# Optimization experiments

Measured on AMD Instinct MI355X. Metric: run time of the kernel, lower is better.

Reference implementation:

```python
import jax, jax.numpy as jnp
import numpy as np

PS = 2      # patch_size
TOPK = 3    # topk


def setup_inputs() -> dict:
    key = jax.random.key(0)
    x = jax.random.normal(key, (8, 128, 64, 64), dtype=jnp.float32)
    alpha = jnp.asarray(5.0, dtype=jnp.float32)  # nn.Parameter alpha
    return {"x": x, "alpha": alpha}


def _forward(x, alpha):
    ps = PS
    b, c, h, w = x.shape
    nph, npw = h // ps, w // ps
    npatch = nph * npw
    pa = ps * ps
    # F.normalize(p=2, dim=-3) with torch eps=1e-12
    norm = jnp.maximum(jnp.sqrt(jnp.sum(x * x, axis=1, keepdims=True)), 1e-12)
    x = x / norm
    # patchify -> [b, c, npatch, patch_area] (patches h-major, pixels row-major)
    xp = x.reshape(b, c, nph, ps, npw, ps).transpose(0, 1, 2, 4, 3, 5)
    xp = xp.reshape(b, c, npatch, pa)
    diag_idx = jnp.arange(ps) * (ps + 1)  # [0, 3] for ps=2
    # gather diagonal pixels of each patch -> [b, ps, npatch, c]
    xd = xp[:, :, :, diag_idx].transpose(0, 3, 2, 1)
    # patch correlation matmul -> [b, ps, npatch, npatch]
    corr = jnp.einsum('bpnc,bpmc->bpnm', xd, xd)
    avg = jnp.mean(corr, axis=1, keepdims=True)
    s = jnp.concatenate([corr, avg], axis=1)  # [b, ps+1, npatch, npatch]
    # ZeroWindow gaussian mask (rat_s=0.05); channel index = patch center (r,c)
    sr, sc = 0.05 * nph, 0.05 * npw
    rr = jnp.arange(nph, dtype=jnp.float32)
    cc = jnp.arange(npw, dtype=jnp.float32)
    cent_r, cent_c = jnp.meshgrid(rr, cc, indexing='ij')
    cent_r = cent_r.reshape(npatch)
    cent_c = cent_c.reshape(npatch)
    gr = jnp.exp(-(rr[None, :] - cent_r[:, None]) ** 2 / (2.0 * sr * sr))  # [npatch, nph]
    gc = jnp.exp(-(cc[None, :] - cent_c[:, None]) ** 2 / (2.0 * sc * sc))  # [npatch, npw]
    mask = (1.0 - gr[:, :, None] * gc[:, None, :]).reshape(npatch, npatch)
    s = s * mask[None, None]
    a = s * alpha
    # double (row + col) softmax
    s = jax.nn.softmax(a, axis=-1) * jax.nn.softmax(a, axis=-2)
    # expand avg channel to all patch pixels, scatter diagonal channels back
    new_x = jnp.broadcast_to(s[:, -1:], (b, pa, npatch, npatch))
    new_x = new_x.at[:, diag_idx].set(s[:, :ps])
    # un-patchify second npatch axis to spatial [b, npatch, h, w]
    y = jnp.swapaxes(new_x, 1, 3)  # [b, npatch, npatch, pa]
    y = y.reshape(b, npatch, nph, npw, ps, ps).transpose(0, 1, 2, 4, 3, 5)
    y = y.reshape(b, npatch, h, w)
    # topk over the npatch axis (dim=-3)
    vals = jax.lax.top_k(jnp.moveaxis(y, 1, -1), TOPK)[0]  # [b, h, w, k]
    return jnp.moveaxis(vals, -1, 1)  # [b, k, h, w]


def reference(x, alpha):
    return _forward(x, alpha)
```

## Files before the change

kernel.cpp:

```cpp
#include <hip/hip_runtime.h>
#include <hip/hip_bf16.h>
#include <math.h>

#define NB 8
#define NC 128
#define NH 64
#define NW 64
#define NP 1024
#define TWO_SIG2 5.12f
#define LOG2E 1.44269504089f

static const size_t PSUM_OFF_B = 0;
static const size_t PBUF_OFF_B = (size_t)NB * 3 * 4 * NP * 4;
static const size_t XD_OFF_B   = PBUF_OFF_B + (size_t)NB * NP * 3 * 4 * 3 * 4;

typedef __bf16 bf16x8 __attribute__((ext_vector_type(8)));
typedef float f32x4 __attribute__((ext_vector_type(4)));

#define INSERT3(v, A, Bq, Cq)                          \
  {                                                    \
    const float _na = fmaxf(A, (v));                   \
    const float _nb = __builtin_amdgcn_fmed3f(A, Bq, (v)); \
    Cq = __builtin_amdgcn_fmed3f(Bq, Cq, (v));         \
    A = _na;                                           \
    Bq = _nb;                                          \
  }

#define MERGE3(a0, a1, a2, b0, b1, b2)       \
  {                                          \
    const float _x1 = fmaxf(a0, b0);         \
    const float _y1 = fminf(a0, b0);         \
    const float _x2 = fmaxf(a1, b1);         \
    const float _z  = fmaxf(a2, b2);         \
    a0 = _x1;                                \
    a1 = fmaxf(_y1, _x2);                    \
    a2 = fmaxf(fminf(_y1, _x2), _z);         \
  }

__global__ __launch_bounds__(256) void k1_norm(const float* __restrict__ x,
                                               __hip_bfloat16* __restrict__ xd) {
  __shared__ __align__(16) float tile[NC * 65];
  const int chunk = blockIdx.x;
  const int p = blockIdx.y;
  const int b = blockIdx.z;
  const int t = threadIdx.x;
  const int pix = t & 63;
  const int cw = t >> 6;
  const int nbase = chunk * 64;

  {
    const int n = nbase + pix;
    const int i = ((n >> 5) << 1) + p;
    const int jf = (n & 31);
    const float* xb = x + (size_t)b * NC * NH * NW + (size_t)i * NW;
    for (int cc = 0; cc < 32; ++cc) {
      const int c = (cc << 2) + cw;
      const float2 v2 = ((const float2*)(xb + (size_t)c * NH * NW))[jf];
      tile[c * 65 + pix] = (p == 0) ? v2.x : v2.y;
    }
  }
  __syncthreads();

  const int lane = t & 63;
  const int w = t >> 6;
  for (int pg = 0; pg < 16; ++pg) {
    const int pixel = (pg << 2) + w;
    const float v0 = tile[lane * 65 + pixel];
    const float v1 = tile[(lane + 64) * 65 + pixel];
    float ss = v0 * v0 + v1 * v1;
#pragma unroll
    for (int m = 32; m >= 1; m >>= 1) ss += __shfl_xor(ss, m, 64);
    const float inv = 1.0f / fmaxf(sqrtf(ss), 1e-12f);
    __hip_bfloat16* xr = xd + ((size_t)((b * 2 + p) * NP) + nbase + pixel) * NC;
    xr[lane] = __float2bfloat16(v0 * inv);
    xr[lane + 64] = __float2bfloat16(v1 * inv);
  }
}

__global__ __launch_bounds__(256) void k2_sums(const ushort* __restrict__ xd,
                                               const float* __restrict__ alpha_p,
                                               float* __restrict__ psum) {
  __shared__ __align__(16) __bf16 As[2][64 * 136];
  __shared__ __align__(16) __bf16 Bs[2][64 * 136];
  const int t = threadIdx.x;
  const float K = (*alpha_p) * LOG2E;
  const float Cm = -(LOG2E / TWO_SIG2);

  const int cchunk = blockIdx.x;
  const int rowtile = blockIdx.y;
  const int b = blockIdx.z;
  const int i0 = rowtile << 6;
  const int jb = cchunk << 8;

#pragma unroll
  for (int pl = 0; pl < 2; ++pl) {
    const float4* ga = (const float4*)(xd + ((size_t)(b * 2 + pl) * NP + i0) * NC);
#pragma unroll
    for (int it = 0; it < 4; ++it) {
      const int f = (it << 8) + t;
      const int r = f >> 4, q = f & 15;
      *(float4*)(&As[pl][r * 136 + q * 8]) = ga[f];
    }
  }

  const int wave = t >> 6;
  const int lane = t & 63;
  const int lrow = lane & 15;
  const int kq = lane >> 4;

  const int n0 = i0 + wave * 16 + kq * 4;
  const float rnf = (float)(n0 >> 5);
  const float cn0 = (float)(n0 & 31);

  float sums[3][4];
#pragma unroll
  for (int ch = 0; ch < 3; ++ch)
#pragma unroll
    for (int reg = 0; reg < 4; ++reg) sums[ch][reg] = 0.f;

  for (int sc = 0; sc < 4; ++sc) {
    const int j0 = jb + (sc << 6);
    __syncthreads();
#pragma unroll
    for (int pl = 0; pl < 2; ++pl) {
      const float4* gb = (const float4*)(xd + ((size_t)(b * 2 + pl) * NP + j0) * NC);
#pragma unroll
      for (int it = 0; it < 4; ++it) {
        const int f = (it << 8) + t;
        const int r = f >> 4, q = f & 15;
        *(float4*)(&Bs[pl][r * 136 + q * 8]) = gb[f];
      }
    }
    __syncthreads();

    f32x4 acc[2][4];
#pragma unroll
    for (int pl = 0; pl < 2; ++pl)
#pragma unroll
      for (int ct = 0; ct < 4; ++ct)
#pragma unroll
        for (int u = 0; u < 4; ++u) acc[pl][ct][u] = 0.f;

#pragma unroll
    for (int kc = 0; kc < 4; ++kc) {
      const int kk = kc * 32 + (kq << 3);
      const bf16x8 a0 = *(const bf16x8*)(&As[0][(wave * 16 + lrow) * 136 + kk]);
      const bf16x8 a1 = *(const bf16x8*)(&As[1][(wave * 16 + lrow) * 136 + kk]);
#pragma unroll
      for (int ct = 0; ct < 4; ++ct) {
        const bf16x8 b0 = *(const bf16x8*)(&Bs[0][(ct * 16 + lrow) * 136 + kk]);
        const bf16x8 b1 = *(const bf16x8*)(&Bs[1][(ct * 16 + lrow) * 136 + kk]);
        acc[0][ct] = __builtin_amdgcn_mfma_f32_16x16x32_bf16(a0, b0, acc[0][ct], 0, 0, 0);
        acc[1][ct] = __builtin_amdgcn_mfma_f32_16x16x32_bf16(a1, b1, acc[1][ct], 0, 0, 0);
      }
    }

#pragma unroll
    for (int ct = 0; ct < 4; ++ct) {
      const int m = j0 + ct * 16 + lrow;
      const float rmf = (float)(m >> 5);
      const float cmf = (float)(m & 31);
      const float dr = rnf - rmf;
      const float dr2 = dr * dr;
#pragma unroll
      for (int reg = 0; reg < 4; ++reg) {
        const float dc = cn0 + (float)reg - cmf;
        const float d2 = fmaf(dc, dc, dr2);
        const float em = __builtin_amdgcn_exp2f(d2 * Cm);
        const float fm2 = fmaf(-em, K, K);
        const float g0 = fm2 * acc[0][ct][reg];
        const float g1 = fm2 * acc[1][ct][reg];
        sums[0][reg] += __builtin_amdgcn_exp2f(g0);
        sums[1][reg] += __builtin_amdgcn_exp2f(g1);
        sums[2][reg] += __builtin_amdgcn_exp2f(0.5f * (g0 + g1));
      }
    }
  }

#pragma unroll
  for (int off = 1; off < 16; off <<= 1)
#pragma unroll
    for (int ch = 0; ch < 3; ++ch)
#pragma unroll
      for (int reg = 0; reg < 4; ++reg)
        sums[ch][reg] += __shfl_xor(sums[ch][reg], off, 64);

  if (lrow == 0) {
#pragma unroll
    for (int ch = 0; ch < 3; ++ch)
#pragma unroll
      for (int reg = 0; reg < 4; ++reg) {
        const int n = i0 + wave * 16 + kq * 4 + reg;
        psum[(((size_t)b * 3 + ch) * 4 + cchunk) * NP + n] = sums[ch][reg];
      }
  }
}

__global__ __launch_bounds__(256) void k4_topk(const ushort* __restrict__ xd,
                                               const float* __restrict__ alpha_p,
                                               const float* __restrict__ psum,
                                               float* __restrict__ pbuf) {
  __shared__ __align__(16) __bf16 As[2][64 * 136];
  __shared__ __align__(16) __bf16 Bs[2][64 * 136];
  __shared__ float rsr[3][64];
  __shared__ float nlc[3][256];
  const int t = threadIdx.x;
  const float K = (*alpha_p) * LOG2E;
  const float Cm = -(LOG2E / TWO_SIG2);

  const int cchunk = blockIdx.x;
  const int rowtile = blockIdx.y;
  const int b = blockIdx.z;
  const int i0 = rowtile << 6;
  const int jb = cchunk << 8;

  if (t < 192) {
    const int ch = t >> 6, r = t & 63;
    const float* pp = psum + ((size_t)b * 3 + ch) * 4 * NP + i0 + r;
    rsr[ch][r] = 1.0f / (pp[0] + pp[NP] + pp[2 * NP] + pp[3 * NP]);
  }
#pragma unroll
  for (int ch = 0; ch < 3; ++ch) {
    const float* pp = psum + ((size_t)b * 3 + ch) * 4 * NP + jb + t;
    nlc[ch][t] = -__builtin_amdgcn_logf(pp[0] + pp[NP] + pp[2 * NP] + pp[3 * NP]);
  }

#pragma unroll
  for (int pl = 0; pl < 2; ++pl) {
    const float4* ga = (const float4*)(xd + ((size_t)(b * 2 + pl) * NP + i0) * NC);
#pragma unroll
    for (int it = 0; it < 4; ++it) {
      const int f = (it << 8) + t;
      const int r = f >> 4, q = f & 15;
      *(float4*)(&As[pl][r * 136 + q * 8]) = ga[f];
    }
  }

  const int wave = t >> 6;
  const int lane = t & 63;
  const int lrow = lane & 15;
  const int kq = lane >> 4;

  const int n0 = i0 + wave * 16 + kq * 4;
  const float rnf = (float)(n0 >> 5);
  const float cn0 = (float)(n0 & 31);

  float tA[3][4], tB[3][4], tC[3][4];
#pragma unroll
  for (int ch = 0; ch < 3; ++ch)
#pragma unroll
    for (int reg = 0; reg < 4; ++reg) {
      tA[ch][reg] = -3.0e38f; tB[ch][reg] = -3.0e38f; tC[ch][reg] = -3.0e38f;
    }

  for (int sc = 0; sc < 4; ++sc) {
    const int j0 = jb + (sc << 6);
    __syncthreads();
#pragma unroll
    for (int pl = 0; pl < 2; ++pl) {
      const float4* gb = (const float4*)(xd + ((size_t)(b * 2 + pl) * NP + j0) * NC);
#pragma unroll
      for (int it = 0; it < 4; ++it) {
        const int f = (it << 8) + t;
        const int r = f >> 4, q = f & 15;
        *(float4*)(&Bs[pl][r * 136 + q * 8]) = gb[f];
      }
    }
    __syncthreads();

    f32x4 acc[2][4];
#pragma unroll
    for (int pl = 0; pl < 2; ++pl)
#pragma unroll
      for (int ct = 0; ct < 4; ++ct)
#pragma unroll
        for (int u = 0; u < 4; ++u) acc[pl][ct][u] = 0.f;

#pragma unroll
    for (int kc = 0; kc < 4; ++kc) {
      const int kk = kc * 32 + (kq << 3);
      const bf16x8 a0 = *(const bf16x8*)(&As[0][(wave * 16 + lrow) * 136 + kk]);
      const bf16x8 a1 = *(const bf16x8*)(&As[1][(wave * 16 + lrow) * 136 + kk]);
#pragma unroll
      for (int ct = 0; ct < 4; ++ct) {
        const bf16x8 b0 = *(const bf16x8*)(&Bs[0][(ct * 16 + lrow) * 136 + kk]);
        const bf16x8 b1 = *(const bf16x8*)(&Bs[1][(ct * 16 + lrow) * 136 + kk]);
        acc[0][ct] = __builtin_amdgcn_mfma_f32_16x16x32_bf16(a0, b0, acc[0][ct], 0, 0, 0);
        acc[1][ct] = __builtin_amdgcn_mfma_f32_16x16x32_bf16(a1, b1, acc[1][ct], 0, 0, 0);
      }
    }

#pragma unroll
    for (int ct = 0; ct < 4; ++ct) {
      const int mc = sc * 64 + ct * 16 + lrow;
      const int m = jb + mc;
      const float rmf = (float)(m >> 5);
      const float cmf = (float)(m & 31);
      const float dr = rnf - rmf;
      const float dr2 = dr * dr;
      const float nl0 = nlc[0][mc];
      const float nl1 = nlc[1][mc];
      const float nl2 = nlc[2][mc];
#pragma unroll
      for (int reg = 0; reg < 4; ++reg) {
        const float dc = cn0 + (float)reg - cmf;
        const float d2 = fmaf(dc, dc, dr2);
        const float em = __builtin_amdgcn_exp2f(d2 * Cm);
        const float fm2 = fmaf(-em, K, K);
        const float f2 = fm2 + fm2;
        const float a0 = acc[0][ct][reg];
        const float a1 = acc[1][ct][reg];
        const float t0 = fmaf(f2, a0, nl0);
        const float t1 = fmaf(f2, a1, nl1);
        const float t2 = fmaf(fm2, a0 + a1, nl2);
        INSERT3(t0, tA[0][reg], tB[0][reg], tC[0][reg]);
        INSERT3(t1, tA[1][reg], tB[1][reg], tC[1][reg]);
        INSERT3(t2, tA[2][reg], tB[2][reg], tC[2][reg]);
      }
    }
  }

#pragma unroll
  for (int off = 1; off < 16; off <<= 1)
#pragma unroll
    for (int ch = 0; ch < 3; ++ch)
#pragma unroll
      for (int reg = 0; reg < 4; ++reg) {
        const float b0 = __shfl_xor(tA[ch][reg], off, 64);
        const float b1 = __shfl_xor(tB[ch][reg], off, 64);
        const float b2 = __shfl_xor(tC[ch][reg], off, 64);
        MERGE3(tA[ch][reg], tB[ch][reg], tC[ch][reg], b0, b1, b2);
      }

  if (lrow == 0) {
#pragma unroll
    for (int ch = 0; ch < 3; ++ch)
#pragma unroll
      for (int reg = 0; reg < 4; ++reg) {
        const int nr = wave * 16 + kq * 4 + reg;
        const int n = i0 + nr;
        const float irn = rsr[ch][nr];
        const size_t base = ((((size_t)b * NP + n) * 3 + ch) * 4 + cchunk) * 3;
        pbuf[base + 0] = __builtin_amdgcn_exp2f(tA[ch][reg]) * irn;
        pbuf[base + 1] = __builtin_amdgcn_exp2f(tB[ch][reg]) * irn;
        pbuf[base + 2] = __builtin_amdgcn_exp2f(tC[ch][reg]) * irn;
      }
  }
}

__global__ __launch_bounds__(256) void k5_merge(const float* __restrict__ pbuf,
                                                float* __restrict__ out) {
  const int tau = blockIdx.x * 256 + threadIdx.x;
  const int b = tau >> 10;
  const int n = tau & (NP - 1);
  const int rn = n >> 5, cn = n & 31;

  float f0[3], f1[3], f2[3];
#pragma unroll
  for (int ch = 0; ch < 3; ++ch) {
    const size_t base = (((size_t)tau * 3 + ch) * 4) * 3;
    f0[ch] = pbuf[base + 0];
    f1[ch] = pbuf[base + 1];
    f2[ch] = pbuf[base + 2];
#pragma unroll
    for (int p = 1; p < 4; ++p) {
      const float b0 = pbuf[base + p * 3 + 0];
      const float b1 = pbuf[base + p * 3 + 1];
      const float b2 = pbuf[base + p * 3 + 2];
      MERGE3(f0[ch], f1[ch], f2[ch], b0, b1, b2);
    }
  }

  float* ob = out + (size_t)b * 3 * (NH * NW);
  const int i00 = ((rn << 1) * NW) + (cn << 1);
#pragma unroll
  for (int tt = 0; tt < 3; ++tt) {
    float* op = ob + (size_t)tt * (NH * NW);
    const float r0 = (tt == 0) ? f0[0] : (tt == 1) ? f1[0] : f2[0];
    const float r1 = (tt == 0) ? f0[1] : (tt == 1) ? f1[1] : f2[1];
    const float r2 = (tt == 0) ? f0[2] : (tt == 1) ? f1[2] : f2[2];
    op[i00] = r0;
    op[i00 + NW + 1] = r1;
    op[i00 + 1] = r2;
    op[i00 + NW] = r2;
  }
}

extern "C" void kernel_launch(void* const* d_in, const int* in_sizes, int n_in,
                              void* d_out, int out_size, void* d_ws, size_t ws_size,
                              hipStream_t stream) {
  const float* x = (const float*)d_in[0];
  const float* alpha = (const float*)d_in[1];
  float* out = (float*)d_out;
  char* ws = (char*)d_ws;

  float* psum = (float*)(ws + PSUM_OFF_B);
  float* pbuf = (float*)(ws + PBUF_OFF_B);
  __hip_bfloat16* xd = (__hip_bfloat16*)(ws + XD_OFF_B);

  k1_norm<<<dim3(16, 2, NB), 256, 0, stream>>>(x, xd);
  k2_sums<<<dim3(4, 16, NB), 256, 0, stream>>>((const ushort*)xd, alpha, psum);
  k4_topk<<<dim3(4, 16, NB), 256, 0, stream>>>((const ushort*)xd, alpha, psum, pbuf);
  k5_merge<<<dim3(32), 256, 0, stream>>>(pbuf, out);
}
```

Baseline: 104.7 us.

## Fuse softmax-sum and topk kernels with grid barrier, keep logits in registers

Merges the row-sum kernel and the topk kernel into one persistent launch. A software grid-wide atomic barrier separates the phases, and each block keeps its masked correlation logits for the second phase in registers (128 floats per thread), so the bf16 GEMM and mask exponentials are not recomputed and the B tiles are not reloaded. This removes a launch and half the MFMA/exp work. The cost is much higher register pressure under launch_bounds(256,2), and the barrier depends on all 512 blocks being co-resident, which is what the bounded spin-timeout guards against.

```diff
diff --git a/kernel.cpp b/kernel.cpp
--- a/kernel.cpp
+++ b/kernel.cpp
@@ -9,10 +9,12 @@
 #define NP 1024
 #define TWO_SIG2 5.12f
 #define LOG2E 1.44269504089f
+#define NBLK 512u
 
 static const size_t PSUM_OFF_B = 0;
 static const size_t PBUF_OFF_B = (size_t)NB * 3 * 4 * NP * 4;
 static const size_t XD_OFF_B   = PBUF_OFF_B + (size_t)NB * NP * 3 * 4 * 3 * 4;
+static const size_t BAR_OFF_B  = XD_OFF_B + (size_t)NB * 2 * NP * NC * 2;
 
 typedef __bf16 bf16x8 __attribute__((ext_vector_type(8)));
 typedef float f32x4 __attribute__((ext_vector_type(4)));
@@ -38,12 +40,16 @@
   }
 
 __global__ __launch_bounds__(256) void k1_norm(const float* __restrict__ x,
-                                               __hip_bfloat16* __restrict__ xd) {
+                                               __hip_bfloat16* __restrict__ xd,
+                                               unsigned* __restrict__ bar) {
   __shared__ __align__(16) float tile[NC * 65];
   const int chunk = blockIdx.x;
   const int p = blockIdx.y;
   const int b = blockIdx.z;
   const int t = threadIdx.x;
+  if (chunk == 0 && p == 0 && b == 0 && t == 0) {
+    __hip_atomic_store(bar, 0u, __ATOMIC_RELAXED, __HIP_MEMORY_SCOPE_AGENT);
+  }
   const int pix = t & 63;
   const int cw = t >> 6;
   const int nbase = chunk * 64;
@@ -77,129 +83,11 @@
   }
 }
 
-__global__ __launch_bounds__(256) void k2_sums(const ushort* __restrict__ xd,
-                                               const float* __restrict__ alpha_p,
-                                               float* __restrict__ psum) {
-  __shared__ __align__(16) __bf16 As[2][64 * 136];
-  __shared__ __align__(16) __bf16 Bs[2][64 * 136];
-  const int t = threadIdx.x;
-  const float K = (*alpha_p) * LOG2E;
-  const float Cm = -(LOG2E / TWO_SIG2);
-
-  const int cchunk = blockIdx.x;
-  const int rowtile = blockIdx.y;
-  const int b = blockIdx.z;
-  const int i0 = rowtile << 6;
-  const int jb = cchunk << 8;
-
-#pragma unroll
-  for (int pl = 0; pl < 2; ++pl) {
-    const float4* ga = (const float4*)(xd + ((size_t)(b * 2 + pl) * NP + i0) * NC);
-#pragma unroll
-    for (int it = 0; it < 4; ++it) {
-      const int f = (it << 8) + t;
-      const int r = f >> 4, q = f & 15;
-      *(float4*)(&As[pl][r * 136 + q * 8]) = ga[f];
-    }
-  }
-
-  const int wave = t >> 6;
-  const int lane = t & 63;
-  const int lrow = lane & 15;
-  const int kq = lane >> 4;
-
-  const int n0 = i0 + wave * 16 + kq * 4;
-  const float rnf = (float)(n0 >> 5);
-  const float cn0 = (float)(n0 & 31);
-
-  float sums[3][4];
-#pragma unroll
-  for (int ch = 0; ch < 3; ++ch)
-#pragma unroll
-    for (int reg = 0; reg < 4; ++reg) sums[ch][reg] = 0.f;
-
-  for (int sc = 0; sc < 4; ++sc) {
-    const int j0 = jb + (sc << 6);
-    __syncthreads();
-#pragma unroll
-    for (int pl = 0; pl < 2; ++pl) {
-      const float4* gb = (const float4*)(xd + ((size_t)(b * 2 + pl) * NP + j0) * NC);
-#pragma unroll
-      for (int it = 0; it < 4; ++it) {
-        const int f = (it << 8) + t;
-        const int r = f >> 4, q = f & 15;
-        *(float4*)(&Bs[pl][r * 136 + q * 8]) = gb[f];
-      }
-    }
-    __syncthreads();
-
-    f32x4 acc[2][4];
-#pragma unroll
-    for (int pl = 0; pl < 2; ++pl)
-#pragma unroll
-      for (int ct = 0; ct < 4; ++ct)
-#pragma unroll
-        for (int u = 0; u < 4; ++u) acc[pl][ct][u] = 0.f;
-
-#pragma unroll
-    for (int kc = 0; kc < 4; ++kc) {
-      const int kk = kc * 32 + (kq << 3);
-      const bf16x8 a0 = *(const bf16x8*)(&As[0][(wave * 16 + lrow) * 136 + kk]);
-      const bf16x8 a1 = *(const bf16x8*)(&As[1][(wave * 16 + lrow) * 136 + kk]);
-#pragma unroll
-      for (int ct = 0; ct < 4; ++ct) {
-        const bf16x8 b0 = *(const bf16x8*)(&Bs[0][(ct * 16 + lrow) * 136 + kk]);
-        const bf16x8 b1 = *(const bf16x8*)(&Bs[1][(ct * 16 + lrow) * 136 + kk]);
-        acc[0][ct] = __builtin_amdgcn_mfma_f32_16x16x32_bf16(a0, b0, acc[0][ct], 0, 0, 0);
-        acc[1][ct] = __builtin_amdgcn_mfma_f32_16x16x32_bf16(a1, b1, acc[1][ct], 0, 0, 0);
-      }
-    }
-
-#pragma unroll
-    for (int ct = 0; ct < 4; ++ct) {
-      const int m = j0 + ct * 16 + lrow;
-      const float rmf = (float)(m >> 5);
-      const float cmf = (float)(m & 31);
-      const float dr = rnf - rmf;
-      const float dr2 = dr * dr;
-#pragma unroll
-      for (int reg = 0; reg < 4; ++reg) {
-        const float dc = cn0 + (float)reg - cmf;
-        const float d2 = fmaf(dc, dc, dr2);
-        const float em = __builtin_amdgcn_exp2f(d2 * Cm);
-        const float fm2 = fmaf(-em, K, K);
-        const float g0 = fm2 * acc[0][ct][reg];
-        const float g1 = fm2 * acc[1][ct][reg];
-        sums[0][reg] += __builtin_amdgcn_exp2f(g0);
-        sums[1][reg] += __builtin_amdgcn_exp2f(g1);
-        sums[2][reg] += __builtin_amdgcn_exp2f(0.5f * (g0 + g1));
-      }
-    }
-  }
-
-#pragma unroll
-  for (int off = 1; off < 16; off <<= 1)
-#pragma unroll
-    for (int ch = 0; ch < 3; ++ch)
-#pragma unroll
-      for (int reg = 0; reg < 4; ++reg)
-        sums[ch][reg] += __shfl_xor(sums[ch][reg], off, 64);
-
-  if (lrow == 0) {
-#pragma unroll
-    for (int ch = 0; ch < 3; ++ch)
-#pragma unroll
-      for (int reg = 0; reg < 4; ++reg) {
-        const int n = i0 + wave * 16 + kq * 4 + reg;
-        psum[(((size_t)b * 3 + ch) * 4 + cchunk) * NP + n] = sums[ch][reg];
-      }
-  }
-}
-
-__global__ __launch_bounds__(256) void k4_topk(const ushort* __restrict__ xd,
-                                               const float* __restrict__ alpha_p,
-                                               const float* __restrict__ psum,
-                                               float* __restrict__ pbuf) {
+__global__ __launch_bounds__(256, 2) void k24_fused(const ushort* __restrict__ xd,
+                                                    const float* __restrict__ alpha_p,
+                                                    float* __restrict__ psum,
+                                                    float* __restrict__ pbuf,
+                                                    unsigned* __restrict__ bar) {
   __shared__ __align__(16) __bf16 As[2][64 * 136];
   __shared__ __align__(16) __bf16 Bs[2][64 * 136];
   __shared__ float rsr[3][64];
@@ -214,6 +102,126 @@
   const int i0 = rowtile << 6;
   const int jb = cchunk << 8;
 
+#pragma unroll
+  for (int pl = 0; pl < 2; ++pl) {
+    const float4* ga = (const float4*)(xd + ((size_t)(b * 2 + pl) * NP + i0) * NC);
+#pragma unroll
+    for (int it = 0; it < 4; ++it) {
+      const int f = (it << 8) + t;
+      const int r = f >> 4, q = f & 15;
+      *(float4*)(&As[pl][r * 136 + q * 8]) = ga[f];
+    }
+  }
+
+  const int wave = t >> 6;
+  const int lane = t & 63;
+  const int lrow = lane & 15;
+  const int kq = lane >> 4;
+
+  const int n0 = i0 + wave * 16 + kq * 4;
+  const float rnf = (float)(n0 >> 5);
+  const float cn0 = (float)(n0 & 31);
+
+  f32x4 g0v[4][4];
+  f32x4 g1v[4][4];
+#pragma unroll
+  for (int sc = 0; sc < 4; ++sc)
+#pragma unroll
+    for (int ct = 0; ct < 4; ++ct)
+#pragma unroll
+      for (int u = 0; u < 4; ++u) { g0v[sc][ct][u] = 0.f; g1v[sc][ct][u] = 0.f; }
+
+  float sums[3][4];
+#pragma unroll
+  for (int ch = 0; ch < 3; ++ch)
+#pragma unroll
+    for (int reg = 0; reg < 4; ++reg) sums[ch][reg] = 0.f;
+
+#pragma unroll
+  for (int sc = 0; sc < 4; ++sc) {
+    const int j0 = jb + (sc << 6);
+    __syncthreads();
+#pragma unroll
+    for (int pl = 0; pl < 2; ++pl) {
+      const float4* gb = (const float4*)(xd + ((size_t)(b * 2 + pl) * NP + j0) * NC);
+#pragma unroll
+      for (int it = 0; it < 4; ++it) {
+        const int f = (it << 8) + t;
+        const int r = f >> 4, q = f & 15;
+        *(float4*)(&Bs[pl][r * 136 + q * 8]) = gb[f];
+      }
+    }
+    __syncthreads();
+
+#pragma unroll
+    for (int kc = 0; kc < 4; ++kc) {
+      const int kk = kc * 32 + (kq << 3);
+      const bf16x8 a0 = *(const bf16x8*)(&As[0][(wave * 16 + lrow) * 136 + kk]);
+      const bf16x8 a1 = *(const bf16x8*)(&As[1][(wave * 16 + lrow) * 136 + kk]);
+#pragma unroll
+      for (int ct = 0; ct < 4; ++ct) {
+        const bf16x8 b0 = *(const bf16x8*)(&Bs[0][(ct * 16 + lrow) * 136 + kk]);
+        const bf16x8 b1 = *(const bf16x8*)(&Bs[1][(ct * 16 + lrow) * 136 + kk]);
+        g0v[sc][ct] = __builtin_amdgcn_mfma_f32_16x16x32_bf16(a0, b0, g0v[sc][ct], 0, 0, 0);
+        g1v[sc][ct] = __builtin_amdgcn_mfma_f32_16x16x32_bf16(a1, b1, g1v[sc][ct], 0, 0, 0);
+      }
+    }
+
+#pragma unroll
+    for (int ct = 0; ct < 4; ++ct) {
+      const int m = j0 + ct * 16 + lrow;
+      const float rmf = (float)(m >> 5);
+      const float cmf = (float)(m & 31);
+      const float dr = rnf - rmf;
+      const float dr2 = dr * dr;
+#pragma unroll
+      for (int reg = 0; reg < 4; ++reg) {
+        const float dc = cn0 + (float)reg - cmf;
+        const float d2 = fmaf(dc, dc, dr2);
+        const float em = __builtin_amdgcn_exp2f(d2 * Cm);
+        const float fm2 = fmaf(-em, K, K);
+        const float g0 = fm2 * g0v[sc][ct][reg];
+        const float g1 = fm2 * g1v[sc][ct][reg];
+        g0v[sc][ct][reg] = g0;
+        g1v[sc][ct][reg] = g1;
+        sums[0][reg] += __builtin_amdgcn_exp2f(g0);
+        sums[1][reg] += __builtin_amdgcn_exp2f(g1);
+        sums[2][reg] += __builtin_amdgcn_exp2f(0.5f * (g0 + g1));
+      }
+    }
+  }
+
+#pragma unroll
+  for (int off = 1; off < 16; off <<= 1)
+#pragma unroll
+    for (int ch = 0; ch < 3; ++ch)
+#pragma unroll
+      for (int reg = 0; reg < 4; ++reg)
+        sums[ch][reg] += __shfl_xor(sums[ch][reg], off, 64);
+
+  if (lrow == 0) {
+#pragma unroll
+    for (int ch = 0; ch < 3; ++ch)
+#pragma unroll
+      for (int reg = 0; reg < 4; ++reg) {
+        const int n = i0 + wave * 16 + kq * 4 + reg;
+        psum[(((size_t)b * 3 + ch) * 4 + cchunk) * NP + n] = sums[ch][reg];
+      }
+  }
+
+  __syncthreads();
+  if (t == 0) {
+    __threadfence();
+    __hip_atomic_fetch_add(bar, 1u, __ATOMIC_ACQ_REL, __HIP_MEMORY_SCOPE_AGENT);
+    long spin = 0;
+    while (__hip_atomic_load(bar, __ATOMIC_ACQUIRE, __HIP_MEMORY_SCOPE_AGENT) < NBLK) {
+      __builtin_amdgcn_s_sleep(8);
+      if (++spin > (1L << 22)) break;
+    }
+    __threadfence();
+  }
+  __syncthreads();
+
   if (t < 192) {
     const int ch = t >> 6, r = t & 63;
     const float* pp = psum + ((size_t)b * 3 + ch) * 4 * NP + i0 + r;
@@ -224,26 +232,7 @@
     const float* pp = psum + ((size_t)b * 3 + ch) * 4 * NP + jb + t;
     nlc[ch][t] = -__builtin_amdgcn_logf(pp[0] + pp[NP] + pp[2 * NP] + pp[3 * NP]);
   }
-
-#pragma unroll
-  for (int pl = 0; pl < 2; ++pl) {
-    const float4* ga = (const float4*)(xd + ((size_t)(b * 2 + pl) * NP + i0) * NC);
-#pragma unroll
-    for (int it = 0; it < 4; ++it) {
-      const int f = (it << 8) + t;
-      const int r = f >> 4, q = f & 15;
-      *(float4*)(&As[pl][r * 136 + q * 8]) = ga[f];
-    }
-  }
-
-  const int wave = t >> 6;
-  const int lane = t & 63;
-  const int lrow = lane & 15;
-  const int kq = lane >> 4;
-
-  const int n0 = i0 + wave * 16 + kq * 4;
-  const float rnf = (float)(n0 >> 5);
-  const float cn0 = (float)(n0 & 31);
+  __syncthreads();
 
   float tA[3][4], tB[3][4], tC[3][4];
 #pragma unroll
@@ -253,66 +242,21 @@
       tA[ch][reg] = -3.0e38f; tB[ch][reg] = -3.0e38f; tC[ch][reg] = -3.0e38f;
     }
 
+#pragma unroll
   for (int sc = 0; sc < 4; ++sc) {
-    const int j0 = jb + (sc << 6);
-    __syncthreads();
-#pragma unroll
-    for (int pl = 0; pl < 2; ++pl) {
-      const float4* gb = (const float4*)(xd + ((size_t)(b * 2 + pl) * NP + j0) * NC);
-#pragma unroll
-      for (int it = 0; it < 4; ++it) {
-        const int f = (it << 8) + t;
-        const int r = f >> 4, q = f & 15;
-        *(float4*)(&Bs[pl][r * 136 + q * 8]) = gb[f];
-      }
-    }
-    __syncthreads();
-
-    f32x4 acc[2][4];
-#pragma unroll
-    for (int pl = 0; pl < 2; ++pl)
-#pragma unroll
-      for (int ct = 0; ct < 4; ++ct)
-#pragma unroll
-        for (int u = 0; u < 4; ++u) acc[pl][ct][u] = 0.f;
-
-#pragma unroll
-    for (int kc = 0; kc < 4; ++kc) {
-      const int kk = kc * 32 + (kq << 3);
-      const bf16x8 a0 = *(const bf16x8*)(&As[0][(wave * 16 + lrow) * 136 + kk]);
-      const bf16x8 a1 = *(const bf16x8*)(&As[1][(wave * 16 + lrow) * 136 + kk]);
-#pragma unroll
-      for (int ct = 0; ct < 4; ++ct) {
-        const bf16x8 b0 = *(const bf16x8*)(&Bs[0][(ct * 16 + lrow) * 136 + kk]);
-        const bf16x8 b1 = *(const bf16x8*)(&Bs[1][(ct * 16 + lrow) * 136 + kk]);
-        acc[0][ct] = __builtin_amdgcn_mfma_f32_16x16x32_bf16(a0, b0, acc[0][ct], 0, 0, 0);
-        acc[1][ct] = __builtin_amdgcn_mfma_f32_16x16x32_bf16(a1, b1, acc[1][ct], 0, 0, 0);
-      }
-    }
-
 #pragma unroll
     for (int ct = 0; ct < 4; ++ct) {
-      const int mc = sc * 64 + ct * 16 + lrow;
-      const int m = jb + mc;
-      const float rmf = (float)(m >> 5);
-      const float cmf = (float)(m & 31);
-      const float dr = rnf - rmf;
-      const float dr2 = dr * dr;
+      const int mc = (sc << 6) + ct * 16 + lrow;
       const float nl0 = nlc[0][mc];
       const float nl1 = nlc[1][mc];
       const float nl2 = nlc[2][mc];
 #pragma unroll
       for (int reg = 0; reg < 4; ++reg) {
-        const float dc = cn0 + (float)reg - cmf;
-        const float d2 = fmaf(dc, dc, dr2);
-        const float em = __builtin_amdgcn_exp2f(d2 * Cm);
-        const float fm2 = fmaf(-em, K, K);
-        const float f2 = fm2 + fm2;
-        const float a0 = acc[0][ct][reg];
-        const float a1 = acc[1][ct][reg];
-        const float t0 = fmaf(f2, a0, nl0);
-        const float t1 = fmaf(f2, a1, nl1);
-        const float t2 = fmaf(fm2, a0 + a1, nl2);
+        const float g0 = g0v[sc][ct][reg];
+        const float g1 = g1v[sc][ct][reg];
+        const float t0 = fmaf(2.0f, g0, nl0);
+        const float t1 = fmaf(2.0f, g1, nl1);
+        const float t2 = (g0 + g1) + nl2;
         INSERT3(t0, tA[0][reg], tB[0][reg], tC[0][reg]);
         INSERT3(t1, tA[1][reg], tB[1][reg], tC[1][reg]);
         INSERT3(t2, tA[2][reg], tB[2][reg], tC[2][reg]);
@@ -397,9 +341,9 @@
   float* psum = (float*)(ws + PSUM_OFF_B);
   float* pbuf = (float*)(ws + PBUF_OFF_B);
   __hip_bfloat16* xd = (__hip_bfloat16*)(ws + XD_OFF_B);
-
-  k1_norm<<<dim3(16, 2, NB), 256, 0, stream>>>(x, xd);
-  k2_sums<<<dim3(4, 16, NB), 256, 0, stream>>>((const ushort*)xd, alpha, psum);
-  k4_topk<<<dim3(4, 16, NB), 256, 0, stream>>>((const ushort*)xd, alpha, psum, pbuf);
+  unsigned* bar = (unsigned*)(ws + BAR_OFF_B);
+
+  k1_norm<<<dim3(16, 2, NB), 256, 0, stream>>>(x, xd, bar);
+  k24_fused<<<dim3(4, 16, NB), 256, 0, stream>>>((const ushort*)xd, alpha, psum, pbuf, bar);
   k5_merge<<<dim3(32), 256, 0, stream>>>(pbuf, out);
 }
```

Result: slower. 145.1 us (+38.6%).

## Load MFMA operands directly from global memory instead of staging through LDS

Applied to the files above, without the earlier changes.

Both correlation kernels stop staging the A and B bf16 tiles in shared memory. Each lane now keeps its A fragments in registers for the whole block and reads B fragments straight from global memory, relying on L1/L2 to serve the reuse across waves. This removes the per-chunk barriers and the LDS write/read traffic, and the smaller LDS footprint may allow more blocks per CU. In exchange, B data is fetched redundantly by all four waves, and the 16-byte global loads are strided by row, so they may coalesce worse and expose more latency.

```diff
diff --git a/kernel.cpp b/kernel.cpp
--- a/kernel.cpp
+++ b/kernel.cpp
@@ -80,8 +80,6 @@
 __global__ __launch_bounds__(256) void k2_sums(const ushort* __restrict__ xd,
                                                const float* __restrict__ alpha_p,
                                                float* __restrict__ psum) {
-  __shared__ __align__(16) __bf16 As[2][64 * 136];
-  __shared__ __align__(16) __bf16 Bs[2][64 * 136];
   const int t = threadIdx.x;
   const float K = (*alpha_p) * LOG2E;
   const float Cm = -(LOG2E / TWO_SIG2);
@@ -92,22 +90,26 @@
   const int i0 = rowtile << 6;
   const int jb = cchunk << 8;
 
-#pragma unroll
-  for (int pl = 0; pl < 2; ++pl) {
-    const float4* ga = (const float4*)(xd + ((size_t)(b * 2 + pl) * NP + i0) * NC);
-#pragma unroll
-    for (int it = 0; it < 4; ++it) {
-      const int f = (it << 8) + t;
-      const int r = f >> 4, q = f & 15;
-      *(float4*)(&As[pl][r * 136 + q * 8]) = ga[f];
-    }
-  }
-
   const int wave = t >> 6;
   const int lane = t & 63;
   const int lrow = lane & 15;
   const int kq = lane >> 4;
 
+  const __bf16* X = (const __bf16*)xd;
+  const __bf16* xp0 = X + ((size_t)(b * 2 + 0) * NP) * NC;
+  const __bf16* xp1 = X + ((size_t)(b * 2 + 1) * NP) * NC;
+
+  bf16x8 a0[4], a1[4];
+  {
+    const __bf16* pa0 = xp0 + (size_t)(i0 + wave * 16 + lrow) * NC + kq * 8;
+    const __bf16* pa1 = xp1 + (size_t)(i0 + wave * 16 + lrow) * NC + kq * 8;
+#pragma unroll
+    for (int kc = 0; kc < 4; ++kc) {
+      a0[kc] = *(const bf16x8*)(pa0 + kc * 32);
+      a1[kc] = *(const bf16x8*)(pa1 + kc * 32);
+    }
+  }
+
   const int n0 = i0 + wave * 16 + kq * 4;
   const float rnf = (float)(n0 >> 5);
   const float cn0 = (float)(n0 & 31);
@@ -120,18 +122,8 @@
 
   for (int sc = 0; sc < 4; ++sc) {
     const int j0 = jb + (sc << 6);
-    __syncthreads();
-#pragma unroll
-    for (int pl = 0; pl < 2; ++pl) {
-      const float4* gb = (const float4*)(xd + ((size_t)(b * 2 + pl) * NP + j0) * NC);
-#pragma unroll
-      for (int it = 0; it < 4; ++it) {
-        const int f = (it << 8) + t;
-        const int r = f >> 4, q = f & 15;
-        *(float4*)(&Bs[pl][r * 136 + q * 8]) = gb[f];
-      }
-    }
-    __syncthreads();
+    const __bf16* pb0 = xp0 + (size_t)(j0 + lrow) * NC + kq * 8;
+    const __bf16* pb1 = xp1 + (size_t)(j0 + lrow) * NC + kq * 8;
 
     f32x4 acc[2][4];
 #pragma unroll
@@ -143,15 +135,12 @@
 
 #pragma unroll
     for (int kc = 0; kc < 4; ++kc) {
-      const int kk = kc * 32 + (kq << 3);
-      const bf16x8 a0 = *(const bf16x8*)(&As[0][(wave * 16 + lrow) * 136 + kk]);
-      const bf16x8 a1 = *(const bf16x8*)(&As[1][(wave * 16 + lrow) * 136 + kk]);
 #pragma unroll
       for (int ct = 0; ct < 4; ++ct) {
-        const bf16x8 b0 = *(const bf16x8*)(&Bs[0][(ct * 16 + lrow) * 136 + kk]);
-        const bf16x8 b1 = *(const bf16x8*)(&Bs[1][(ct * 16 + lrow) * 136 + kk]);
-        acc[0][ct] = __builtin_amdgcn_mfma_f32_16x16x32_bf16(a0, b0, acc[0][ct], 0, 0, 0);
-        acc[1][ct] = __builtin_amdgcn_mfma_f32_16x16x32_bf16(a1, b1, acc[1][ct], 0, 0, 0);
+        const bf16x8 b0 = *(const bf16x8*)(pb0 + (size_t)(ct * 16) * NC + kc * 32);
+        const bf16x8 b1 = *(const bf16x8*)(pb1 + (size_t)(ct * 16) * NC + kc * 32);
+        acc[0][ct] = __builtin_amdgcn_mfma_f32_16x16x32_bf16(a0[kc], b0, acc[0][ct], 0, 0, 0);
+        acc[1][ct] = __builtin_amdgcn_mfma_f32_16x16x32_bf16(a1[kc], b1, acc[1][ct], 0, 0, 0);
       }
     }
 
@@ -200,8 +189,6 @@
                                                const float* __restrict__ alpha_p,
                                                const float* __restrict__ psum,
                                                float* __restrict__ pbuf) {
-  __shared__ __align__(16) __bf16 As[2][64 * 136];
-  __shared__ __align__(16) __bf16 Bs[2][64 * 136];
   __shared__ float rsr[3][64];
   __shared__ float nlc[3][256];
   const int t = threadIdx.x;
@@ -225,22 +212,26 @@
     nlc[ch][t] = -__builtin_amdgcn_logf(pp[0] + pp[NP] + pp[2 * NP] + pp[3 * NP]);
   }
 
-#pragma unroll
-  for (int pl = 0; pl < 2; ++pl) {
-    const float4* ga = (const float4*)(xd + ((size_t)(b * 2 + pl) * NP + i0) * NC);
-#pragma unroll
-    for (int it = 0; it < 4; ++it) {
-      const int f = (it << 8) + t;
-      const int r = f >> 4, q = f & 15;
-      *(float4*)(&As[pl][r * 136 + q * 8]) = ga[f];
-    }
-  }
-
   const int wave = t >> 6;
   const int lane = t & 63;
   const int lrow = lane & 15;
   const int kq = lane >> 4;
 
+  const __bf16* X = (const __bf16*)xd;
+  const __bf16* xp0 = X + ((size_t)(b * 2 + 0) * NP) * NC;
+  const __bf16* xp1 = X + ((size_t)(b * 2 + 1) * NP) * NC;
+
+  bf16x8 a0[4], a1[4];
+  {
+    const __bf16* pa0 = xp0 + (size_t)(i0 + wave * 16 + lrow) * NC + kq * 8;
+    const __bf16* pa1 = xp1 + (size_t)(i0 + wave * 16 + lrow) * NC + kq * 8;
+#pragma unroll
+    for (int kc = 0; kc < 4; ++kc) {
+      a0[kc] = *(const bf16x8*)(pa0 + kc * 32);
+      a1[kc] = *(const bf16x8*)(pa1 + kc * 32);
+    }
+  }
+
   const int n0 = i0 + wave * 16 + kq * 4;
   const float rnf = (float)(n0 >> 5);
   const float cn0 = (float)(n0 & 31);
@@ -253,20 +244,12 @@
       tA[ch][reg] = -3.0e38f; tB[ch][reg] = -3.0e38f; tC[ch][reg] = -3.0e38f;
     }
 
+  __syncthreads();
+
   for (int sc = 0; sc < 4; ++sc) {
     const int j0 = jb + (sc << 6);
-    __syncthreads();
-#pragma unroll
-    for (int pl = 0; pl < 2; ++pl) {
-      const float4* gb = (const float4*)(xd + ((size_t)(b * 2 + pl) * NP + j0) * NC);
-#pragma unroll
-      for (int it = 0; it < 4; ++it) {
-        const int f = (it << 8) + t;
-        const int r = f >> 4, q = f & 15;
-        *(float4*)(&Bs[pl][r * 136 + q * 8]) = gb[f];
-      }
-    }
-    __syncthreads();
+    const __bf16* pb0 = xp0 + (size_t)(j0 + lrow) * NC + kq * 8;
+    const __bf16* pb1 = xp1 + (size_t)(j0 + lrow) * NC + kq * 8;
 
     f32x4 acc[2][4];
 #pragma unroll
@@ -278,21 +261,18 @@
 
 #pragma unroll
     for (int kc = 0; kc < 4; ++kc) {
-      const int kk = kc * 32 + (kq << 3);
-      const bf16x8 a0 = *(const bf16x8*)(&As[0][(wave * 16 + lrow) * 136 + kk]);
-      const bf16x8 a1 = *(const bf16x8*)(&As[1][(wave * 16 + lrow) * 136 + kk]);
 #pragma unroll
       for (int ct = 0; ct < 4; ++ct) {
-        const bf16x8 b0 = *(const bf16x8*)(&Bs[0][(ct * 16 + lrow) * 136 + kk]);
-        const bf16x8 b1 = *(const bf16x8*)(&Bs[1][(ct * 16 + lrow) * 136 + kk]);
-        acc[0][ct] = __builtin_amdgcn_mfma_f32_16x16x32_bf16(a0, b0, acc[0][ct], 0, 0, 0);
-        acc[1][ct] = __builtin_amdgcn_mfma_f32_16x16x32_bf16(a1, b1, acc[1][ct], 0, 0, 0);
+        const bf16x8 b0 = *(const bf16x8*)(pb0 + (size_t)(ct * 16) * NC + kc * 32);
+        const bf16x8 b1 = *(const bf16x8*)(pb1 + (size_t)(ct * 16) * NC + kc * 32);
+        acc[0][ct] = __builtin_amdgcn_mfma_f32_16x16x32_bf16(a0[kc], b0, acc[0][ct], 0, 0, 0);
+        acc[1][ct] = __builtin_amdgcn_mfma_f32_16x16x32_bf16(a1[kc], b1, acc[1][ct], 0, 0, 0);
       }
     }
 
 #pragma unroll
     for (int ct = 0; ct < 4; ++ct) {
-      const int mc = sc * 64 + ct * 16 + lrow;
+      const int mc = (sc << 6) + ct * 16 + lrow;
       const int m = jb + mc;
       const float rmf = (float)(m >> 5);
       const float cmf = (float)(m & 31);
@@ -308,11 +288,11 @@
         const float em = __builtin_amdgcn_exp2f(d2 * Cm);
         const float fm2 = fmaf(-em, K, K);
         const float f2 = fm2 + fm2;
-        const float a0 = acc[0][ct][reg];
-        const float a1 = acc[1][ct][reg];
-        const float t0 = fmaf(f2, a0, nl0);
-        const float t1 = fmaf(f2, a1, nl1);
-        const float t2 = fmaf(fm2, a0 + a1, nl2);
+        const float a0v = acc[0][ct][reg];
+        const float a1v = acc[1][ct][reg];
+        const float t0 = fmaf(f2, a0v, nl0);
+        const float t1 = fmaf(f2, a1v, nl1);
+        const float t2 = fmaf(fm2, a0v + a1v, nl2);
         INSERT3(t0, tA[0][reg], tB[0][reg], tC[0][reg]);
         INSERT3(t1, tA[1][reg], tB[1][reg], tC[1][reg]);
         INSERT3(t2, tA[2][reg], tB[2][reg], tC[2][reg]);
```

Result: slower. 147.7 us (+41.1%).
